# Kernel optimization log

Hardware: AMD Instinct MI355X
Metric: run time of the kernel (lower is better)

The kernel has to match this reference:

```python
import jax, jax.numpy as jnp
import numpy as np

SCALE = 2.0   # init scale
OFFSET = 0.5  # init offset
BIG = 1e10    # stand-in for +inf so grads stay finite
N_PAD = 2048  # number of zero-padded pc columns per sample


def setup_inputs() -> dict:
    key = jax.random.key(0)
    k1, k2 = jax.random.split(key)
    vertices = jax.random.normal(k1, (4, 3, 64, 32, 64), dtype=jnp.float32)
    pc = jax.random.normal(k2, (4, 3, 8192), dtype=jnp.float32)
    # zero-pad the tail columns, mimicking variable-length point clouds
    pc = pc.at[:, :, 8192 - N_PAD:].set(0.0)
    return {"vertices": vertices, "pc": pc}


def _chamfer_loss(v, p, mask):
    # v: [N,3] mesh-top points; p: [M,3] cloud points; mask: [M] valid flags
    # squared pairwise distances via ||v||^2 + ||p||^2 - 2 v.p
    d = (jnp.sum(v * v, axis=1)[:, None]
         + jnp.sum(p * p, axis=1)[None, :]
         - 2.0 * (v @ p.T))                      # [N, M]
    dist1 = jnp.min(jnp.where(mask[None, :], d, BIG), axis=1)  # [N] v -> nearest valid p
    dist2 = jnp.min(d, axis=0)                                  # [M] p -> nearest v
    n_valid = jnp.maximum(jnp.sum(mask), 1).astype(d.dtype)
    return jnp.mean(dist1) + jnp.sum(jnp.where(mask, dist2, 0.0)) / n_valid


def reference(vertices, pc):
    B = vertices.shape[0]
    # top surface: last index along dim 3, flattened -> [B, 3, N]
    top = vertices[:, :, :, -1, :].reshape(B, 3, -1)
    top = (top - OFFSET) * SCALE
    v = jnp.transpose(top, (0, 2, 1))   # [B, N, 3]
    p = jnp.transpose(pc, (0, 2, 1))    # [B, M, 3]
    mask = ~jnp.all(pc == 0.0, axis=1)  # [B, M] valid (non-zero-padded) points
    loss = jax.vmap(_chamfer_loss)(v, p, mask)  # [B]
    return jnp.mean(loss)
```

## Files before the change

kernel.cpp:

```cpp
#include <hip/hip_runtime.h>

#define BATCH   4
#define NPTS    4096
#define MPTS    8192
#define TPB     256
#define VPT     8
#define MSPLIT  32
#define NSPLIT  16
#define MLEN    (MPTS / MSPLIT)
#define NLEN    (NPTS / NSPLIT)
#define D1_NBLK (NPTS / (TPB * VPT))
#define D2_MBLK (MPTS / (TPB * VPT))
#define D1_BLOCKS (BATCH * D1_NBLK * MSPLIT)
#define D2_BLOCKS (BATCH * D2_MBLK * NSPLIT)
#define BIGF    1.0e30f

__device__ __forceinline__ float vtop(const float* __restrict__ v, int b, int c, int n) {
    return v[b * 393216 + c * 131072 + ((n >> 6) << 11) + 1984 + (n & 63)];
}

__device__ __forceinline__ void atomicMinF(float* addr, float val) {
    atomicMin((unsigned int*)addr, __float_as_uint(val));
}

__global__ void __launch_bounds__(TPB) dist_kernel(const float* __restrict__ vert,
                                                   const float* __restrict__ pc,
                                                   float* __restrict__ part1,
                                                   float* __restrict__ part2,
                                                   float* __restrict__ dist1f,
                                                   float* __restrict__ dist2f,
                                                   int use_atomic) {
    __shared__ float4 tile[TPB];
    const int tid = threadIdx.x;
    int blk = blockIdx.x;

    if (blk < D1_BLOCKS) {
        const int c  = blk % MSPLIT;
        const int nb = (blk / MSPLIT) % D1_NBLK;
        const int b  = blk / (MSPLIT * D1_NBLK);
        const float* pcb = pc + (size_t)b * 3 * MPTS;

        {
            const int m = c * MLEN + tid;
            const float qx = pcb[m], qy = pcb[MPTS + m], qz = pcb[2 * MPTS + m];
            const bool valid = !(qx == 0.0f && qy == 0.0f && qz == 0.0f);
            const float qn2 = valid ? 0.5f * (qx * qx + qy * qy + qz * qz) : BIGF;
            tile[tid] = make_float4(qx, qy, qz, qn2);
        }

        float vx[VPT], vy[VPT], vz[VPT], best[VPT];
        const int nbase = nb * (TPB * VPT) + tid;
#pragma unroll
        for (int k = 0; k < VPT; ++k) {
            const int n = nbase + k * TPB;
            vx[k] = (vtop(vert, b, 0, n) - 0.5f) * 2.0f;
            vy[k] = (vtop(vert, b, 1, n) - 0.5f) * 2.0f;
            vz[k] = (vtop(vert, b, 2, n) - 0.5f) * 2.0f;
            best[k] = BIGF;
        }
        __syncthreads();

#pragma unroll 4
        for (int j = 0; j < MLEN; ++j) {
            const float4 q = tile[j];
#pragma unroll
            for (int k = 0; k < VPT; ++k) {
                best[k] = fminf(best[k],
                    fmaf(-vx[k], q.x, fmaf(-vy[k], q.y, fmaf(-vz[k], q.z, q.w))));
            }
        }

        if (use_atomic) {
#pragma unroll
            for (int k = 0; k < VPT; ++k) {
                const int n = nbase + k * TPB;
                const float vv = vx[k]*vx[k] + vy[k]*vy[k] + vz[k]*vz[k];
                atomicMinF(&dist1f[b * NPTS + n], fmaxf(vv + 2.0f * best[k], 0.0f));
            }
        } else {
            float* outp = part1 + (size_t)c * (BATCH * NPTS) + (size_t)b * NPTS;
#pragma unroll
            for (int k = 0; k < VPT; ++k) {
                const int n = nbase + k * TPB;
                const float vv = vx[k]*vx[k] + vy[k]*vy[k] + vz[k]*vz[k];
                outp[n] = fmaxf(vv + 2.0f * best[k], 0.0f);
            }
        }
    } else {
        blk -= D1_BLOCKS;
        const int c  = blk % NSPLIT;
        const int mb = (blk / NSPLIT) % D2_MBLK;
        const int b  = blk / (NSPLIT * D2_MBLK);
        const float* pcb = pc + (size_t)b * 3 * MPTS;

        {
            const int n = c * NLEN + tid;
            const float sx = (vtop(vert, b, 0, n) - 0.5f) * 2.0f;
            const float sy = (vtop(vert, b, 1, n) - 0.5f) * 2.0f;
            const float sz = (vtop(vert, b, 2, n) - 0.5f) * 2.0f;
            tile[tid] = make_float4(sx, sy, sz, 0.5f * (sx*sx + sy*sy + sz*sz));
        }

        float qx[VPT], qy[VPT], qz[VPT], best[VPT];
        const int mbase = mb * (TPB * VPT) + tid;
#pragma unroll
        for (int k = 0; k < VPT; ++k) {
            const int m = mbase + k * TPB;
            qx[k] = pcb[m];
            qy[k] = pcb[MPTS + m];
            qz[k] = pcb[2 * MPTS + m];
            best[k] = BIGF;
        }
        __syncthreads();

#pragma unroll 4
        for (int j = 0; j < NLEN; ++j) {
            const float4 t = tile[j];
#pragma unroll
            for (int k = 0; k < VPT; ++k) {
                best[k] = fminf(best[k],
                    fmaf(-qx[k], t.x, fmaf(-qy[k], t.y, fmaf(-qz[k], t.z, t.w))));
            }
        }

        if (use_atomic) {
#pragma unroll
            for (int k = 0; k < VPT; ++k) {
                const int m = mbase + k * TPB;
                const float qq = qx[k]*qx[k] + qy[k]*qy[k] + qz[k]*qz[k];
                atomicMinF(&dist2f[b * MPTS + m], fmaxf(qq + 2.0f * best[k], 0.0f));
            }
        } else {
            float* outp = part2 + (size_t)c * (BATCH * MPTS) + (size_t)b * MPTS;
#pragma unroll
            for (int k = 0; k < VPT; ++k) {
                const int m = mbase + k * TPB;
                const float qq = qx[k]*qx[k] + qy[k]*qy[k] + qz[k]*qz[k];
                outp[m] = fmaxf(qq + 2.0f * best[k], 0.0f);
            }
        }
    }
}

__global__ void __launch_bounds__(TPB) reduce_kernel(const float* __restrict__ part1,
                                                     const float* __restrict__ part2,
                                                     const float* __restrict__ dist1f,
                                                     const float* __restrict__ dist2f,
                                                     const float* __restrict__ pc,
                                                     float* __restrict__ sums,
                                                     int use_atomic) {
    const int gid = blockIdx.x * TPB + threadIdx.x;
    if (gid < BATCH * NPTS) {
        const int b = gid / NPTS;
        float s;
        if (use_atomic) {
            s = dist1f[gid];
        } else {
            float best = BIGF;
#pragma unroll
            for (int c = 0; c < MSPLIT; ++c)
                best = fminf(best, part1[(size_t)c * (BATCH * NPTS) + gid]);
            s = best;
        }
        for (int off = 32; off > 0; off >>= 1) s += __shfl_down(s, off, 64);
        if ((threadIdx.x & 63) == 0) atomicAdd(&sums[b], s);
    } else {
        const int g2 = gid - BATCH * NPTS;
        const int b  = g2 / MPTS;
        const int m  = g2 % MPTS;
        const float* pcb = pc + (size_t)b * 3 * MPTS;
        const float qx = pcb[m], qy = pcb[MPTS + m], qz = pcb[2 * MPTS + m];
        const bool valid = !(qx == 0.0f && qy == 0.0f && qz == 0.0f);
        float s = 0.0f, cn = 0.0f;
        if (valid) {
            if (use_atomic) {
                s = dist2f[g2];
            } else {
                float best = BIGF;
#pragma unroll
                for (int c = 0; c < NSPLIT; ++c)
                    best = fminf(best, part2[(size_t)c * (BATCH * MPTS) + g2]);
                s = best;
            }
            cn = 1.0f;
        }
        for (int off = 32; off > 0; off >>= 1) {
            s  += __shfl_down(s, off, 64);
            cn += __shfl_down(cn, off, 64);
        }
        if ((threadIdx.x & 63) == 0) {
            atomicAdd(&sums[4 + b], s);
            atomicAdd(&sums[8 + b], cn);
        }
    }
}

__global__ void finalize_kernel(const float* __restrict__ sums, float* __restrict__ out) {
    if (blockIdx.x == 0 && threadIdx.x == 0) {
        float t = 0.0f;
        for (int b = 0; b < BATCH; ++b)
            t += sums[b] * (1.0f / (float)NPTS) + sums[4 + b] / fmaxf(sums[8 + b], 1.0f);
        out[0] = t * (1.0f / (float)BATCH);
    }
}

extern "C" void kernel_launch(void* const* d_in, const int* in_sizes, int n_in,
                              void* d_out, int out_size, void* d_ws, size_t ws_size,
                              hipStream_t stream) {
    const float* vert = (const float*)d_in[0];
    const float* pc   = (const float*)d_in[1];
    float* out = (float*)d_out;

    const size_t part1_elems = (size_t)MSPLIT * BATCH * NPTS;
    const size_t part2_elems = (size_t)NSPLIT * BATCH * MPTS;
    const size_t need_partial = (part1_elems + part2_elems + 16) * sizeof(float);

    const int grid_dist   = D1_BLOCKS + D2_BLOCKS;
    const int grid_reduce = (BATCH * (NPTS + MPTS)) / TPB;

    if (ws_size >= need_partial) {
        float* part1 = (float*)d_ws;
        float* part2 = part1 + part1_elems;
        float* sums  = part2 + part2_elems;
        hipMemsetAsync(sums, 0, 16 * sizeof(float), stream);
        dist_kernel<<<grid_dist, TPB, 0, stream>>>(vert, pc, part1, part2, nullptr, nullptr, 0);
        reduce_kernel<<<grid_reduce, TPB, 0, stream>>>(part1, part2, nullptr, nullptr, pc, sums, 0);
        finalize_kernel<<<1, 64, 0, stream>>>(sums, out);
    } else {
        float* dist1f = (float*)d_ws;
        float* dist2f = dist1f + BATCH * NPTS;
        float* sums   = dist2f + BATCH * MPTS;
        hipMemsetAsync(d_ws, 0x7f, (size_t)BATCH * (NPTS + MPTS) * sizeof(float), stream);
        hipMemsetAsync(sums, 0, 16 * sizeof(float), stream);
        dist_kernel<<<grid_dist, TPB, 0, stream>>>(vert, pc, nullptr, nullptr, dist1f, dist2f, 1);
        reduce_kernel<<<grid_reduce, TPB, 0, stream>>>(nullptr, nullptr, dist1f, dist2f, pc, sums, 1);
        finalize_kernel<<<1, 64, 0, stream>>>(sums, out);
    }
}
```

Measured before the change: 99.49 us.

## Fuse finalize into reduce with last-block pattern and drop memset launch

Removes the memset and finalize launches by zeroing the control block inside dist_kernel and having the last reduce block (found via an atomic counter) compute the final loss. The reduce kernel now handles four elements per thread with float4 loads and does a block-level reduction before one atomic per block. The atomic fallback path for small workspaces is dropped, so the code now assumes the workspace is large enough. The intent is to cut launch overhead and atomic contention, at the cost of relying on ctrl[15], whose zeroing goes through a float store, and on the fence ordering between blocks.

```diff
diff --git a/kernel.cpp b/kernel.cpp
--- a/kernel.cpp
+++ b/kernel.cpp
@@ -15,24 +15,29 @@
 #define D2_BLOCKS (BATCH * D2_MBLK * NSPLIT)
 #define BIGF    1.0e30f
 
+#define PART1_ELEMS (MSPLIT * BATCH * NPTS)
+#define PART2_ELEMS (NSPLIT * BATCH * MPTS)
+
+#define R1_BLOCKS ((BATCH * NPTS) / (TPB * 4))
+#define R2_BLOCKS ((BATCH * MPTS) / (TPB * 4))
+#define R_BLOCKS  (R1_BLOCKS + R2_BLOCKS)
+
+#define CTRL_FLOATS 16
+
 __device__ __forceinline__ float vtop(const float* __restrict__ v, int b, int c, int n) {
     return v[b * 393216 + c * 131072 + ((n >> 6) << 11) + 1984 + (n & 63)];
-}
-
-__device__ __forceinline__ void atomicMinF(float* addr, float val) {
-    atomicMin((unsigned int*)addr, __float_as_uint(val));
 }
 
 __global__ void __launch_bounds__(TPB) dist_kernel(const float* __restrict__ vert,
                                                    const float* __restrict__ pc,
                                                    float* __restrict__ part1,
                                                    float* __restrict__ part2,
-                                                   float* __restrict__ dist1f,
-                                                   float* __restrict__ dist2f,
-                                                   int use_atomic) {
+                                                   float* __restrict__ ctrl) {
     __shared__ float4 tile[TPB];
     const int tid = threadIdx.x;
     int blk = blockIdx.x;
+
+    if (blk == 0 && tid < CTRL_FLOATS) ctrl[tid] = 0.0f;
 
     if (blk < D1_BLOCKS) {
         const int c  = blk % MSPLIT;
@@ -70,21 +75,12 @@
             }
         }
 
-        if (use_atomic) {
-#pragma unroll
-            for (int k = 0; k < VPT; ++k) {
-                const int n = nbase + k * TPB;
-                const float vv = vx[k]*vx[k] + vy[k]*vy[k] + vz[k]*vz[k];
-                atomicMinF(&dist1f[b * NPTS + n], fmaxf(vv + 2.0f * best[k], 0.0f));
-            }
-        } else {
-            float* outp = part1 + (size_t)c * (BATCH * NPTS) + (size_t)b * NPTS;
-#pragma unroll
-            for (int k = 0; k < VPT; ++k) {
-                const int n = nbase + k * TPB;
-                const float vv = vx[k]*vx[k] + vy[k]*vy[k] + vz[k]*vz[k];
-                outp[n] = fmaxf(vv + 2.0f * best[k], 0.0f);
-            }
+        float* outp = part1 + (size_t)c * (BATCH * NPTS) + (size_t)b * NPTS;
+#pragma unroll
+        for (int k = 0; k < VPT; ++k) {
+            const int n = nbase + k * TPB;
+            const float vv = vx[k]*vx[k] + vy[k]*vy[k] + vz[k]*vz[k];
+            outp[n] = fmaxf(vv + 2.0f * best[k], 0.0f);
         }
     } else {
         blk -= D1_BLOCKS;
@@ -123,84 +119,90 @@
             }
         }
 
-        if (use_atomic) {
-#pragma unroll
-            for (int k = 0; k < VPT; ++k) {
-                const int m = mbase + k * TPB;
-                const float qq = qx[k]*qx[k] + qy[k]*qy[k] + qz[k]*qz[k];
-                atomicMinF(&dist2f[b * MPTS + m], fmaxf(qq + 2.0f * best[k], 0.0f));
-            }
-        } else {
-            float* outp = part2 + (size_t)c * (BATCH * MPTS) + (size_t)b * MPTS;
-#pragma unroll
-            for (int k = 0; k < VPT; ++k) {
-                const int m = mbase + k * TPB;
-                const float qq = qx[k]*qx[k] + qy[k]*qy[k] + qz[k]*qz[k];
-                outp[m] = fmaxf(qq + 2.0f * best[k], 0.0f);
-            }
+        float* outp = part2 + (size_t)c * (BATCH * MPTS) + (size_t)b * MPTS;
+#pragma unroll
+        for (int k = 0; k < VPT; ++k) {
+            const int m = mbase + k * TPB;
+            const float qq = qx[k]*qx[k] + qy[k]*qy[k] + qz[k]*qz[k];
+            outp[m] = fmaxf(qq + 2.0f * best[k], 0.0f);
         }
     }
 }
 
 __global__ void __launch_bounds__(TPB) reduce_kernel(const float* __restrict__ part1,
                                                      const float* __restrict__ part2,
-                                                     const float* __restrict__ dist1f,
-                                                     const float* __restrict__ dist2f,
                                                      const float* __restrict__ pc,
-                                                     float* __restrict__ sums,
-                                                     int use_atomic) {
-    const int gid = blockIdx.x * TPB + threadIdx.x;
-    if (gid < BATCH * NPTS) {
-        const int b = gid / NPTS;
-        float s;
-        if (use_atomic) {
-            s = dist1f[gid];
+                                                     float* __restrict__ ctrl,
+                                                     float* __restrict__ out) {
+    const int tid = threadIdx.x;
+    const int wid = tid >> 6;
+    __shared__ float rs[4], rc[4];
+
+    float s = 0.0f, cn = 0.0f;
+    int b;
+
+    if (blockIdx.x < R1_BLOCKS) {
+        const int gid = blockIdx.x * (TPB * 4) + tid * 4;
+        b = gid / NPTS;
+        float4 best = make_float4(BIGF, BIGF, BIGF, BIGF);
+#pragma unroll
+        for (int c = 0; c < MSPLIT; ++c) {
+            const float4 v = *(const float4*)&part1[(size_t)c * (BATCH * NPTS) + gid];
+            best.x = fminf(best.x, v.x); best.y = fminf(best.y, v.y);
+            best.z = fminf(best.z, v.z); best.w = fminf(best.w, v.w);
+        }
+        s = best.x + best.y + best.z + best.w;
+    } else {
+        const int g2 = (blockIdx.x - R1_BLOCKS) * (TPB * 4) + tid * 4;
+        b = g2 / MPTS;
+        const int m = g2 % MPTS;
+        float4 best = make_float4(BIGF, BIGF, BIGF, BIGF);
+#pragma unroll
+        for (int c = 0; c < NSPLIT; ++c) {
+            const float4 v = *(const float4*)&part2[(size_t)c * (BATCH * MPTS) + g2];
+            best.x = fminf(best.x, v.x); best.y = fminf(best.y, v.y);
+            best.z = fminf(best.z, v.z); best.w = fminf(best.w, v.w);
+        }
+        const float* pcb = pc + (size_t)b * 3 * MPTS;
+        const float4 qx = *(const float4*)&pcb[m];
+        const float4 qy = *(const float4*)&pcb[MPTS + m];
+        const float4 qz = *(const float4*)&pcb[2 * MPTS + m];
+        const bool v0 = !(qx.x == 0.0f && qy.x == 0.0f && qz.x == 0.0f);
+        const bool v1 = !(qx.y == 0.0f && qy.y == 0.0f && qz.y == 0.0f);
+        const bool v2 = !(qx.z == 0.0f && qy.z == 0.0f && qz.z == 0.0f);
+        const bool v3 = !(qx.w == 0.0f && qy.w == 0.0f && qz.w == 0.0f);
+        s  = (v0 ? best.x : 0.0f) + (v1 ? best.y : 0.0f)
+           + (v2 ? best.z : 0.0f) + (v3 ? best.w : 0.0f);
+        cn = (float)v0 + (float)v1 + (float)v2 + (float)v3;
+    }
+
+    for (int off = 32; off > 0; off >>= 1) {
+        s  += __shfl_down(s, off, 64);
+        cn += __shfl_down(cn, off, 64);
+    }
+    if ((tid & 63) == 0) { rs[wid] = s; rc[wid] = cn; }
+    __syncthreads();
+
+    if (tid == 0) {
+        const float ts = rs[0] + rs[1] + rs[2] + rs[3];
+        if (blockIdx.x < R1_BLOCKS) {
+            atomicAdd(&ctrl[b], ts);
         } else {
-            float best = BIGF;
-#pragma unroll
-            for (int c = 0; c < MSPLIT; ++c)
-                best = fminf(best, part1[(size_t)c * (BATCH * NPTS) + gid]);
-            s = best;
-        }
-        for (int off = 32; off > 0; off >>= 1) s += __shfl_down(s, off, 64);
-        if ((threadIdx.x & 63) == 0) atomicAdd(&sums[b], s);
-    } else {
-        const int g2 = gid - BATCH * NPTS;
-        const int b  = g2 / MPTS;
-        const int m  = g2 % MPTS;
-        const float* pcb = pc + (size_t)b * 3 * MPTS;
-        const float qx = pcb[m], qy = pcb[MPTS + m], qz = pcb[2 * MPTS + m];
-        const bool valid = !(qx == 0.0f && qy == 0.0f && qz == 0.0f);
-        float s = 0.0f, cn = 0.0f;
-        if (valid) {
-            if (use_atomic) {
-                s = dist2f[g2];
-            } else {
-                float best = BIGF;
-#pragma unroll
-                for (int c = 0; c < NSPLIT; ++c)
-                    best = fminf(best, part2[(size_t)c * (BATCH * MPTS) + g2]);
-                s = best;
+            atomicAdd(&ctrl[4 + b], ts);
+            atomicAdd(&ctrl[8 + b], rc[0] + rc[1] + rc[2] + rc[3]);
+        }
+        __threadfence();
+        const unsigned int old = atomicAdd((unsigned int*)&ctrl[15], 1u);
+        if (old == R_BLOCKS - 1) {
+            float t = 0.0f;
+            for (int bb = 0; bb < BATCH; ++bb) {
+                const float s1 = atomicAdd(&ctrl[bb], 0.0f);
+                const float s2 = atomicAdd(&ctrl[4 + bb], 0.0f);
+                const float nv = atomicAdd(&ctrl[8 + bb], 0.0f);
+                t += s1 * (1.0f / (float)NPTS) + s2 / fmaxf(nv, 1.0f);
             }
-            cn = 1.0f;
-        }
-        for (int off = 32; off > 0; off >>= 1) {
-            s  += __shfl_down(s, off, 64);
-            cn += __shfl_down(cn, off, 64);
-        }
-        if ((threadIdx.x & 63) == 0) {
-            atomicAdd(&sums[4 + b], s);
-            atomicAdd(&sums[8 + b], cn);
-        }
-    }
-}
-
-__global__ void finalize_kernel(const float* __restrict__ sums, float* __restrict__ out) {
-    if (blockIdx.x == 0 && threadIdx.x == 0) {
-        float t = 0.0f;
-        for (int b = 0; b < BATCH; ++b)
-            t += sums[b] * (1.0f / (float)NPTS) + sums[4 + b] / fmaxf(sums[8 + b], 1.0f);
-        out[0] = t * (1.0f / (float)BATCH);
+            out[0] = t * (1.0f / (float)BATCH);
+        }
     }
 }
 
@@ -211,29 +213,10 @@
     const float* pc   = (const float*)d_in[1];
     float* out = (float*)d_out;
 
-    const size_t part1_elems = (size_t)MSPLIT * BATCH * NPTS;
-    const size_t part2_elems = (size_t)NSPLIT * BATCH * MPTS;
-    const size_t need_partial = (part1_elems + part2_elems + 16) * sizeof(float);
-
-    const int grid_dist   = D1_BLOCKS + D2_BLOCKS;
-    const int grid_reduce = (BATCH * (NPTS + MPTS)) / TPB;
-
-    if (ws_size >= need_partial) {
-        float* part1 = (float*)d_ws;
-        float* part2 = part1 + part1_elems;
-        float* sums  = part2 + part2_elems;
-        hipMemsetAsync(sums, 0, 16 * sizeof(float), stream);
-        dist_kernel<<<grid_dist, TPB, 0, stream>>>(vert, pc, part1, part2, nullptr, nullptr, 0);
-        reduce_kernel<<<grid_reduce, TPB, 0, stream>>>(part1, part2, nullptr, nullptr, pc, sums, 0);
-        finalize_kernel<<<1, 64, 0, stream>>>(sums, out);
-    } else {
-        float* dist1f = (float*)d_ws;
-        float* dist2f = dist1f + BATCH * NPTS;
-        float* sums   = dist2f + BATCH * MPTS;
-        hipMemsetAsync(d_ws, 0x7f, (size_t)BATCH * (NPTS + MPTS) * sizeof(float), stream);
-        hipMemsetAsync(sums, 0, 16 * sizeof(float), stream);
-        dist_kernel<<<grid_dist, TPB, 0, stream>>>(vert, pc, nullptr, nullptr, dist1f, dist2f, 1);
-        reduce_kernel<<<grid_reduce, TPB, 0, stream>>>(nullptr, nullptr, dist1f, dist2f, pc, sums, 1);
-        finalize_kernel<<<1, 64, 0, stream>>>(sums, out);
-    }
-}
+    float* part1 = (float*)d_ws;
+    float* part2 = part1 + PART1_ELEMS;
+    float* ctrl  = part2 + PART2_ELEMS;
+
+    dist_kernel<<<D1_BLOCKS + D2_BLOCKS, TPB, 0, stream>>>(vert, pc, part1, part2, ctrl);
+    reduce_kernel<<<R_BLOCKS, TPB, 0, stream>>>(part1, part2, pc, ctrl, out);
+}
```

Result: faster. 86.76 us, median of 2 (-12.8%).
